# Kernel tuning notes

Measured on AMD Instinct MI355X. Metric: run time of the kernel, lower is better.

Reference implementation:

```python
import jax, jax.numpy as jnp
import numpy as np

DIM = 1024
HEADS = 16
DIM_HEAD = 64
INNER = HEADS * DIM_HEAD
SEQ = 4096
BATCH = 1


def setup_inputs() -> dict:
    key = jax.random.key(0)
    ks = jax.random.split(key, 6)
    s = 0.02
    return {
        "x": jax.random.normal(ks[0], (BATCH, SEQ, DIM), dtype=jnp.float32),
        "Wq": jax.random.normal(ks[1], (DIM, INNER), dtype=jnp.float32) * s,
        "Wk": jax.random.normal(ks[2], (DIM, INNER), dtype=jnp.float32) * s,
        "Wv": jax.random.normal(ks[3], (DIM, INNER), dtype=jnp.float32) * s,
        "Wo": jax.random.normal(ks[4], (INNER, DIM), dtype=jnp.float32) * s,
        "bo": jax.random.normal(ks[5], (DIM,), dtype=jnp.float32) * s,
    }


def reference(x, Wq, Wk, Wv, Wo, bo):
    b, n, _ = x.shape
    beta = 1.0 / jnp.sqrt(jnp.float32(DIM_HEAD))
    # project and split heads: [b, n, inner] -> [b, h, n, d]
    def split_heads(t):
        return t.reshape(b, n, HEADS, DIM_HEAD).transpose(0, 2, 1, 3)
    q = split_heads(x @ Wq)
    k = split_heads(x @ Wk)
    v = split_heads(x @ Wv)
    # scaled scores [b, h, n, n]
    scores = jnp.einsum('bhid,bhjd->bhij', q * beta, k)
    mask_value = -jnp.finfo(scores.dtype).max
    causal = jnp.triu(jnp.ones((n, n), dtype=bool), k=1)
    scores = jnp.where(causal, mask_value, scores)
    attn = jax.nn.softmax(scores, axis=-1)
    out = jnp.einsum('bhij,bhjd->bhid', attn, v)
    out = out.transpose(0, 2, 1, 3).reshape(b, n, INNER)
    # output projection (dropout is identity in eval)
    return out @ Wo + bo
```

## Files before the change

### kernel.cpp

```cpp
#include <hip/hip_runtime.h>
#include <hip/hip_bf16.h>
#include <stdint.h>
#include <math.h>

#define SEQ 4096
#define DIM 1024
#define NHEADS 16
#define DHEAD 64
#define INNER 1024

typedef __hip_bfloat16 bf16;
typedef __attribute__((ext_vector_type(8))) short short8;
typedef __attribute__((ext_vector_type(4))) float floatx4;

__device__ __forceinline__ void gll16(const bf16* g, bf16* l) {
    __builtin_amdgcn_global_load_lds(
        (const __attribute__((address_space(1))) unsigned int*)g,
        (__attribute__((address_space(3))) unsigned int*)l,
        16, 0, 0);
}

__device__ __forceinline__ unsigned short f2bf_bits(float f) {
    bf16 h = __float2bfloat16(f);
    return *reinterpret_cast<unsigned short*>(&h);
}

__device__ __forceinline__ uint2 pack4bf(float a, float b, float c, float d) {
    __hip_bfloat162 lo = __float22bfloat162_rn(float2{a, b});
    __hip_bfloat162 hi = __float22bfloat162_rn(float2{c, d});
    uint2 r;
    r.x = *reinterpret_cast<unsigned*>(&lo);
    r.y = *reinterpret_cast<unsigned*>(&hi);
    return r;
}

__global__ __launch_bounds__(256) void prep_kernel(
        const float* __restrict__ x, const float* __restrict__ W0,
        const float* __restrict__ W1, const float* __restrict__ W2,
        const float* __restrict__ W3, bf16* __restrict__ xb,
        bf16* __restrict__ T0, bf16* __restrict__ T1,
        bf16* __restrict__ T2, bf16* __restrict__ T3) {
    const int tid = threadIdx.x + threadIdx.y * blockDim.x;
    if (blockIdx.z == 4) {
        int chunk = blockIdx.y * 32 + blockIdx.x;
        int base = chunk * 4096 + tid * 4;
        #pragma unroll
        for (int r = 0; r < 4; r++) {
            int i = base + r * 1024;
            float4 f = *reinterpret_cast<const float4*>(x + i);
            unsigned long long p = (unsigned long long)f2bf_bits(f.x)
                                 | ((unsigned long long)f2bf_bits(f.y) << 16)
                                 | ((unsigned long long)f2bf_bits(f.z) << 32)
                                 | ((unsigned long long)f2bf_bits(f.w) << 48);
            *reinterpret_cast<unsigned long long*>(xb + i) = p;
        }
        return;
    }
    const float* W; bf16* T;
    switch (blockIdx.z) {
        case 0:  W = W0; T = T0; break;
        case 1:  W = W1; T = T1; break;
        case 2:  W = W2; T = T2; break;
        default: W = W3; T = T3; break;
    }
    __shared__ float tile[32][33];
    int k0 = blockIdx.x * 32, n0 = blockIdx.y * 32;
    int tx = threadIdx.x, ty = threadIdx.y;
    #pragma unroll
    for (int i = 0; i < 4; i++)
        tile[ty + 8 * i][tx] = W[(size_t)(k0 + ty + 8 * i) * 1024 + n0 + tx];
    __syncthreads();
    #pragma unroll
    for (int i = 0; i < 4; i++)
        T[(size_t)(n0 + ty + 8 * i) * 1024 + k0 + tx] = __float2bfloat16(tile[tx][ty + 8 * i]);
}

__device__ __forceinline__ void gemm128_body(const bf16* __restrict__ A,
                                             const bf16* __restrict__ Bt,
                                             int m0, int n0, floatx4 acc[4][4]) {
    __shared__ __align__(16) bf16 As[8192];
    __shared__ __align__(16) bf16 Bs[8192];
    const int tid = threadIdx.x;
    const int wave = tid >> 6;
    const int lane = tid & 63;
    const int l15 = lane & 15;
    const int quad = lane >> 4;

    #pragma unroll
    for (int i = 0; i < 4; i++)
        #pragma unroll
        for (int j = 0; j < 4; j++)
            acc[i][j] = (floatx4){0.f, 0.f, 0.f, 0.f};

    for (int k0 = 0; k0 < 1024; k0 += 64) {
        __syncthreads();
        #pragma unroll
        for (int j = 0; j < 4; j++) {
            int t = wave * 4 + j;
            int row = (t >> 1) * 16 + l15;
            int kb = (t & 1) * 32 + quad * 8;
            gll16(A + (size_t)(m0 + row) * 1024 + k0 + kb, &As[t * 512]);
            gll16(Bt + (size_t)(n0 + row) * 1024 + k0 + kb, &Bs[t * 512]);
        }
        __syncthreads();
        #pragma unroll
        for (int ks = 0; ks < 2; ks++) {
            short8 af[4], bfr[4];
            #pragma unroll
            for (int i = 0; i < 4; i++)
                af[i] = *reinterpret_cast<const short8*>(
                    &As[((((wave >> 1) * 4 + i) * 2 + ks) * 512) + lane * 8]);
            #pragma unroll
            for (int j = 0; j < 4; j++)
                bfr[j] = *reinterpret_cast<const short8*>(
                    &Bs[((((wave & 1) * 4 + j) * 2 + ks) * 512) + lane * 8]);
            #pragma unroll
            for (int i = 0; i < 4; i++)
                #pragma unroll
                for (int j = 0; j < 4; j++)
                    acc[i][j] = __builtin_amdgcn_mfma_f32_16x16x32_bf16(af[i], bfr[j], acc[i][j], 0, 0, 0);
        }
    }
}

__global__ __launch_bounds__(256) void qkv_gemm_kernel(
        const bf16* __restrict__ xb,
        const bf16* __restrict__ Wqt, const bf16* __restrict__ Wkt, const bf16* __restrict__ Wvt,
        bf16* __restrict__ Qh, bf16* __restrict__ Kh, bf16* __restrict__ Vt) {
    const bf16* Bt;
    if (blockIdx.z == 0)      Bt = Wqt;
    else if (blockIdx.z == 1) Bt = Wkt;
    else                      Bt = Wvt;
    int n0 = blockIdx.x * 128, m0 = blockIdx.y * 128;
    floatx4 acc[4][4];
    gemm128_body(xb, Bt, m0, n0, acc);

    const int tid = threadIdx.x, wave = tid >> 6, lane = tid & 63;
    const int l15 = lane & 15, quad = lane >> 4;
    const int wm = (wave >> 1) * 64, wn = (wave & 1) * 64;
    if (blockIdx.z == 2) {
        #pragma unroll
        for (int i = 0; i < 4; i++)
            #pragma unroll
            for (int j = 0; j < 4; j++) {
                int col = n0 + wn + j * 16 + l15;
                int h = col >> 6, d = col & 63;
                int row0 = m0 + wm + i * 16 + quad * 4;
                uint2 v = pack4bf(acc[i][j][0], acc[i][j][1], acc[i][j][2], acc[i][j][3]);
                *reinterpret_cast<uint2*>(Vt + ((size_t)h * DHEAD + d) * SEQ + row0) = v;
            }
    } else {
        bf16* O = (blockIdx.z == 0) ? Qh : Kh;
        float scale = (blockIdx.z == 0) ? 0.125f * 1.4426950408889634f : 1.0f;
        #pragma unroll
        for (int i = 0; i < 4; i++)
            #pragma unroll
            for (int j = 0; j < 4; j++) {
                int col = n0 + wn + j * 16 + l15;
                int h = col >> 6, d = col & 63;
                #pragma unroll
                for (int r = 0; r < 4; r++) {
                    int row = m0 + wm + i * 16 + quad * 4 + r;
                    O[((size_t)h * SEQ + row) * DHEAD + d] = __float2bfloat16(acc[i][j][r] * scale);
                }
            }
    }
}

__global__ __launch_bounds__(256) void out_gemm_kernel(
        const bf16* __restrict__ Oa, const bf16* __restrict__ Wot,
        const float* __restrict__ bo, float* __restrict__ out) {
    int n0 = blockIdx.x * 128, m0 = blockIdx.y * 128;
    floatx4 acc[4][4];
    gemm128_body(Oa, Wot, m0, n0, acc);

    const int tid = threadIdx.x, wave = tid >> 6, lane = tid & 63;
    const int l15 = lane & 15, quad = lane >> 4;
    const int wm = (wave >> 1) * 64, wn = (wave & 1) * 64;
    #pragma unroll
    for (int i = 0; i < 4; i++)
        #pragma unroll
        for (int j = 0; j < 4; j++) {
            int col = n0 + wn + j * 16 + l15;
            float b = bo[col];
            #pragma unroll
            for (int r = 0; r < 4; r++) {
                int row = m0 + wm + i * 16 + quad * 4 + r;
                out[(size_t)row * DIM + col] = acc[i][j][r] + b;
            }
        }
}

__global__ __launch_bounds__(256, 4) void attention_kernel(
        const bf16* __restrict__ Qh, const bf16* __restrict__ Kh,
        const bf16* __restrict__ Vt, bf16* __restrict__ Oa,
        float* __restrict__ Op0, float* __restrict__ Op1,
        float* __restrict__ L0, float* __restrict__ L1) {
    __shared__ __align__(16) bf16 Ksh[2][4096];
    __shared__ __align__(16) bf16 Vsh[2][4096];
    __shared__ __align__(16) bf16 Ps[4][1024];
    const int tid = threadIdx.x, wave = tid >> 6, lane = tid & 63;
    const int l15 = lane & 15, quad = lane >> 4;
    const int id = blockIdx.x;
    const int head = id & 15;
    const int rk = id >> 4;
    int qt, ck;
    if (rk < 32) { qt = 32 + rk; ck = 0; }
    else {
        int j = rk - 32, pair = j >> 1;
        if ((j & 1) == 0) { qt = 63 - pair; ck = 1; }
        else              { qt = 31 - pair; ck = 0; }
    }
    const int ktile0 = ck ? 32 : 0;
    const int ktile1 = (qt < 32) ? (qt + 1) : (ck ? (qt + 1) : 32);
    const int qw = qt * 64 + wave * 16;
    const size_t hoff = (size_t)head * SEQ * DHEAD;
    const bf16* Qb = Qh + hoff;
    const bf16* Kb = Kh + hoff;
    const bf16* Vb = Vt + hoff;

    short8 bq[2];
    #pragma unroll
    for (int s = 0; s < 2; s++)
        bq[s] = *reinterpret_cast<const short8*>(
            Qb + (size_t)(qw + l15) * DHEAD + s * 32 + quad * 8);

    floatx4 acc_o[4];
    #pragma unroll
    for (int c = 0; c < 4; c++) acc_o[c] = (floatx4){0.f, 0.f, 0.f, 0.f};
    float l_part = 0.f;

    auto stage = [&](int buf, int kbase) {
        #pragma unroll
        for (int j = 0; j < 2; j++) {
            int t = wave * 2 + j;
            gll16(Kb + (size_t)(kbase + (t >> 1) * 16 + l15) * DHEAD + (t & 1) * 32 + quad * 8,
                  &Ksh[buf][t * 512]);
            gll16(Vb + (size_t)((t >> 1) * 16 + l15) * SEQ + kbase + (t & 1) * 32 + quad * 8,
                  &Vsh[buf][t * 512]);
        }
    };

    stage(0, ktile0 * 64);
    __syncthreads();
    int cur = 0;
    for (int kt = ktile0; kt < ktile1; kt++) {
        const int kbase = kt * 64;
        if (kt + 1 < ktile1) stage(cur ^ 1, (kt + 1) * 64);

        floatx4 st[4];
        #pragma unroll
        for (int c = 0; c < 4; c++) st[c] = (floatx4){0.f, 0.f, 0.f, 0.f};
        __builtin_amdgcn_s_setprio(1);
        #pragma unroll
        for (int c = 0; c < 4; c++) {
            short8 ak0 = *reinterpret_cast<const short8*>(&Ksh[cur][(c * 2 + 0) * 512 + lane * 8]);
            short8 ak1 = *reinterpret_cast<const short8*>(&Ksh[cur][(c * 2 + 1) * 512 + lane * 8]);
            st[c] = __builtin_amdgcn_mfma_f32_16x16x32_bf16(ak0, bq[0], st[c], 0, 0, 0);
            st[c] = __builtin_amdgcn_mfma_f32_16x16x32_bf16(ak1, bq[1], st[c], 0, 0, 0);
        }
        __builtin_amdgcn_s_setprio(0);
        if (kbase + 63 > qw) {
            int base0 = kbase + quad * 4 - qw - l15;
            #pragma unroll
            for (int c = 0; c < 4; c++) {
                int base = base0 + c * 16;
                #pragma unroll
                for (int r = 0; r < 4; r++)
                    if (base + r > 0) st[c][r] = -1e30f;
            }
        }
        #pragma unroll
        for (int c = 0; c < 4; c++) {
            float p0 = __builtin_amdgcn_exp2f(st[c][0]);
            float p1 = __builtin_amdgcn_exp2f(st[c][1]);
            float p2 = __builtin_amdgcn_exp2f(st[c][2]);
            float p3 = __builtin_amdgcn_exp2f(st[c][3]);
            l_part += (p0 + p1) + (p2 + p3);
            int elem = (c >> 1) * 512
                     + (l15 + 16 * ((c & 1) * 2 + (quad >> 1))) * 8 + (quad & 1) * 4;
            *reinterpret_cast<uint2*>(&Ps[wave][elem]) = pack4bf(p0, p1, p2, p3);
        }
        __builtin_amdgcn_s_setprio(1);
        #pragma unroll
        for (int s = 0; s < 2; s++) {
            short8 bp = *reinterpret_cast<const short8*>(&Ps[wave][s * 512 + lane * 8]);
            #pragma unroll
            for (int c = 0; c < 4; c++) {
                short8 av = *reinterpret_cast<const short8*>(&Vsh[cur][(c * 2 + s) * 512 + lane * 8]);
                acc_o[c] = __builtin_amdgcn_mfma_f32_16x16x32_bf16(av, bp, acc_o[c], 0, 0, 0);
            }
        }
        __builtin_amdgcn_s_setprio(0);

        __syncthreads();
        cur ^= 1;
    }
    float l = l_part;
    l += __shfl_xor(l, 16, 64);
    l += __shfl_xor(l, 32, 64);
    const int q = qw + l15;
    if (qt < 32) {
        float rcp = 1.0f / l;
        #pragma unroll
        for (int c = 0; c < 4; c++) {
            uint2 v = pack4bf(acc_o[c][0] * rcp, acc_o[c][1] * rcp,
                              acc_o[c][2] * rcp, acc_o[c][3] * rcp);
            *reinterpret_cast<uint2*>(Oa + (size_t)q * INNER + head * DHEAD + c * 16 + quad * 4) = v;
        }
    } else {
        float* Op = ck ? Op1 : Op0;
        float* Lp = ck ? L1 : L0;
        if (quad == 0) Lp[head * 2048 + (q - 2048)] = l;
        #pragma unroll
        for (int c = 0; c < 4; c++)
            *reinterpret_cast<floatx4*>(
                Op + (size_t)(q - 2048) * INNER + head * DHEAD + c * 16 + quad * 4) = acc_o[c];
    }
}

__global__ __launch_bounds__(256) void combine_kernel(
        const float* __restrict__ Op0, const float* __restrict__ Op1,
        const float* __restrict__ L0, const float* __restrict__ L1,
        bf16* __restrict__ Oa) {
    int idx = blockIdx.x * 256 + threadIdx.x;
    int row = idx >> 8;
    int c4 = (idx & 255) * 4;
    int head = c4 >> 6;
    float l = L0[head * 2048 + row] + L1[head * 2048 + row];
    float rcp = 1.0f / l;
    float4 a = *reinterpret_cast<const float4*>(Op0 + (size_t)row * INNER + c4);
    float4 b = *reinterpret_cast<const float4*>(Op1 + (size_t)row * INNER + c4);
    uint2 v = pack4bf((a.x + b.x) * rcp, (a.y + b.y) * rcp,
                      (a.z + b.z) * rcp, (a.w + b.w) * rcp);
    *reinterpret_cast<uint2*>(Oa + (size_t)(2048 + row) * INNER + c4) = v;
}

extern "C" void kernel_launch(void* const* d_in, const int* in_sizes, int n_in,
                              void* d_out, int out_size, void* d_ws, size_t ws_size,
                              hipStream_t stream) {
    const float* x  = (const float*)d_in[0];
    const float* Wq = (const float*)d_in[1];
    const float* Wk = (const float*)d_in[2];
    const float* Wv = (const float*)d_in[3];
    const float* Wo = (const float*)d_in[4];
    const float* bo = (const float*)d_in[5];
    float* out = (float*)d_out;

    char* ws = (char*)d_ws;
    size_t off = 0;
    bf16* xb  = (bf16*)(ws + off); off += (size_t)SEQ * DIM * 2;
    bf16* Wqt = (bf16*)(ws + off); off += (size_t)DIM * INNER * 2;
    bf16* Wkt = (bf16*)(ws + off); off += (size_t)DIM * INNER * 2;
    bf16* Wvt = (bf16*)(ws + off); off += (size_t)DIM * INNER * 2;
    bf16* Wot = (bf16*)(ws + off); off += (size_t)INNER * DIM * 2;
    bf16* Qh  = (bf16*)(ws + off); off += (size_t)NHEADS * SEQ * DHEAD * 2;
    bf16* Kh  = (bf16*)(ws + off); off += (size_t)NHEADS * SEQ * DHEAD * 2;
    bf16* Vtr = (bf16*)(ws + off); off += (size_t)NHEADS * DHEAD * SEQ * 2;
    bf16* Oa  = (bf16*)(ws + off); off += (size_t)SEQ * INNER * 2;
    float* Op0 = (float*)(ws + off); off += (size_t)(SEQ / 2) * INNER * 4;
    float* Op1 = (float*)(ws + off); off += (size_t)(SEQ / 2) * INNER * 4;
    float* L0  = (float*)(ws + off); off += (size_t)NHEADS * (SEQ / 2) * 4;
    float* L1  = (float*)(ws + off); off += (size_t)NHEADS * (SEQ / 2) * 4;

    prep_kernel<<<dim3(32, 32, 5), dim3(32, 8), 0, stream>>>(x, Wq, Wk, Wv, Wo,
                                                             xb, Wqt, Wkt, Wvt, Wot);
    qkv_gemm_kernel<<<dim3(8, 32, 3), 256, 0, stream>>>(xb, Wqt, Wkt, Wvt, Qh, Kh, Vtr);
    attention_kernel<<<1536, 256, 0, stream>>>(Qh, Kh, Vtr, Oa, Op0, Op1, L0, L1);
    combine_kernel<<<2048, 256, 0, stream>>>(Op0, Op1, L0, L1, Oa);
    out_gemm_kernel<<<dim3(8, 32), 256, 0, stream>>>(Oa, Wot, bo, out);
}
```

Measured before the change: 249.9 us.

## Split attention waves into 2 query groups x 2 key halves with LDS reduction

Each wave now handles 32 query rows (two 16-row groups) against half of the 64-key tile, instead of 16 rows against all 64 keys. Each K and V fragment loaded from LDS now feeds two MFMAs, halving LDS read traffic per MFMA for the score and PV products. The cost is partial O and l accumulators that must be summed across key-half wave pairs at the end through shared memory with extra barriers, plus higher register use from doubled accumulators.

```diff
diff --git a/kernel.cpp b/kernel.cpp
--- a/kernel.cpp
+++ b/kernel.cpp
@@ -196,11 +196,14 @@
         const bf16* __restrict__ Vt, bf16* __restrict__ Oa,
         float* __restrict__ Op0, float* __restrict__ Op1,
         float* __restrict__ L0, float* __restrict__ L1) {
-    __shared__ __align__(16) bf16 Ksh[2][4096];
-    __shared__ __align__(16) bf16 Vsh[2][4096];
-    __shared__ __align__(16) bf16 Ps[4][1024];
+    __shared__ __align__(16) char smem[40960];
+    bf16* Kshb = (bf16*)smem;
+    bf16* Vshb = (bf16*)(smem + 16384);
+    bf16* Psb  = (bf16*)(smem + 32768);
     const int tid = threadIdx.x, wave = tid >> 6, lane = tid & 63;
     const int l15 = lane & 15, quad = lane >> 4;
+    const int kp = wave & 1;
+    const int pr = wave >> 1;
     const int id = blockIdx.x;
     const int head = id & 15;
     const int rk = id >> 4;
@@ -213,31 +216,35 @@
     }
     const int ktile0 = ck ? 32 : 0;
     const int ktile1 = (qt < 32) ? (qt + 1) : (ck ? (qt + 1) : 32);
-    const int qw = qt * 64 + wave * 16;
+    const int qw = qt * 64 + pr * 32;
     const size_t hoff = (size_t)head * SEQ * DHEAD;
     const bf16* Qb = Qh + hoff;
     const bf16* Kb = Kh + hoff;
     const bf16* Vb = Vt + hoff;
 
-    short8 bq[2];
-    #pragma unroll
-    for (int s = 0; s < 2; s++)
-        bq[s] = *reinterpret_cast<const short8*>(
-            Qb + (size_t)(qw + l15) * DHEAD + s * 32 + quad * 8);
-
-    floatx4 acc_o[4];
-    #pragma unroll
-    for (int c = 0; c < 4; c++) acc_o[c] = (floatx4){0.f, 0.f, 0.f, 0.f};
-    float l_part = 0.f;
+    short8 bq[2][2];
+    #pragma unroll
+    for (int g = 0; g < 2; g++)
+        #pragma unroll
+        for (int s = 0; s < 2; s++)
+            bq[g][s] = *reinterpret_cast<const short8*>(
+                Qb + (size_t)(qw + g * 16 + l15) * DHEAD + s * 32 + quad * 8);
+
+    floatx4 acc_o[2][4];
+    #pragma unroll
+    for (int g = 0; g < 2; g++)
+        #pragma unroll
+        for (int c = 0; c < 4; c++) acc_o[g][c] = (floatx4){0.f, 0.f, 0.f, 0.f};
+    float l_part[2] = {0.f, 0.f};
 
     auto stage = [&](int buf, int kbase) {
         #pragma unroll
         for (int j = 0; j < 2; j++) {
             int t = wave * 2 + j;
             gll16(Kb + (size_t)(kbase + (t >> 1) * 16 + l15) * DHEAD + (t & 1) * 32 + quad * 8,
-                  &Ksh[buf][t * 512]);
+                  &Kshb[buf * 4096 + t * 512]);
             gll16(Vb + (size_t)((t >> 1) * 16 + l15) * SEQ + kbase + (t & 1) * 32 + quad * 8,
-                  &Vsh[buf][t * 512]);
+                  &Vshb[buf * 4096 + t * 512]);
         }
     };
 
@@ -248,47 +255,59 @@
         const int kbase = kt * 64;
         if (kt + 1 < ktile1) stage(cur ^ 1, (kt + 1) * 64);
 
-        floatx4 st[4];
-        #pragma unroll
-        for (int c = 0; c < 4; c++) st[c] = (floatx4){0.f, 0.f, 0.f, 0.f};
+        floatx4 st[2][2];
+        #pragma unroll
+        for (int g = 0; g < 2; g++)
+            #pragma unroll
+            for (int kg = 0; kg < 2; kg++) st[g][kg] = (floatx4){0.f, 0.f, 0.f, 0.f};
         __builtin_amdgcn_s_setprio(1);
         #pragma unroll
-        for (int c = 0; c < 4; c++) {
-            short8 ak0 = *reinterpret_cast<const short8*>(&Ksh[cur][(c * 2 + 0) * 512 + lane * 8]);
-            short8 ak1 = *reinterpret_cast<const short8*>(&Ksh[cur][(c * 2 + 1) * 512 + lane * 8]);
-            st[c] = __builtin_amdgcn_mfma_f32_16x16x32_bf16(ak0, bq[0], st[c], 0, 0, 0);
-            st[c] = __builtin_amdgcn_mfma_f32_16x16x32_bf16(ak1, bq[1], st[c], 0, 0, 0);
+        for (int kg = 0; kg < 2; kg++) {
+            short8 ak0 = *reinterpret_cast<const short8*>(
+                &Kshb[cur * 4096 + ((kp * 2 + kg) * 2 + 0) * 512 + lane * 8]);
+            short8 ak1 = *reinterpret_cast<const short8*>(
+                &Kshb[cur * 4096 + ((kp * 2 + kg) * 2 + 1) * 512 + lane * 8]);
+            st[0][kg] = __builtin_amdgcn_mfma_f32_16x16x32_bf16(ak0, bq[0][0], st[0][kg], 0, 0, 0);
+            st[0][kg] = __builtin_amdgcn_mfma_f32_16x16x32_bf16(ak1, bq[0][1], st[0][kg], 0, 0, 0);
+            st[1][kg] = __builtin_amdgcn_mfma_f32_16x16x32_bf16(ak0, bq[1][0], st[1][kg], 0, 0, 0);
+            st[1][kg] = __builtin_amdgcn_mfma_f32_16x16x32_bf16(ak1, bq[1][1], st[1][kg], 0, 0, 0);
         }
         __builtin_amdgcn_s_setprio(0);
-        if (kbase + 63 > qw) {
-            int base0 = kbase + quad * 4 - qw - l15;
+        #pragma unroll
+        for (int g = 0; g < 2; g++) {
+            if (kbase + kp * 32 + 31 > qw + g * 16) {
+                int base0 = kbase + kp * 32 + quad * 4 - (qw + g * 16) - l15;
+                #pragma unroll
+                for (int kg = 0; kg < 2; kg++) {
+                    int base = base0 + kg * 16;
+                    #pragma unroll
+                    for (int r = 0; r < 4; r++)
+                        if (base + r > 0) st[g][kg][r] = -1e30f;
+                }
+            }
+        }
+        #pragma unroll
+        for (int g = 0; g < 2; g++)
+            #pragma unroll
+            for (int kg = 0; kg < 2; kg++) {
+                float p0 = __builtin_amdgcn_exp2f(st[g][kg][0]);
+                float p1 = __builtin_amdgcn_exp2f(st[g][kg][1]);
+                float p2 = __builtin_amdgcn_exp2f(st[g][kg][2]);
+                float p3 = __builtin_amdgcn_exp2f(st[g][kg][3]);
+                l_part[g] += (p0 + p1) + (p2 + p3);
+                int elem = g * 512 + (l15 + 16 * (kg * 2 + (quad >> 1))) * 8 + (quad & 1) * 4;
+                *reinterpret_cast<uint2*>(&Psb[wave * 1024 + elem]) = pack4bf(p0, p1, p2, p3);
+            }
+        __builtin_amdgcn_s_setprio(1);
+        {
+            short8 bp0 = *reinterpret_cast<const short8*>(&Psb[wave * 1024 + 0 * 512 + lane * 8]);
+            short8 bp1 = *reinterpret_cast<const short8*>(&Psb[wave * 1024 + 1 * 512 + lane * 8]);
             #pragma unroll
             for (int c = 0; c < 4; c++) {
-                int base = base0 + c * 16;
-                #pragma unroll
-                for (int r = 0; r < 4; r++)
-                    if (base + r > 0) st[c][r] = -1e30f;
-            }
-        }
-        #pragma unroll
-        for (int c = 0; c < 4; c++) {
-            float p0 = __builtin_amdgcn_exp2f(st[c][0]);
-            float p1 = __builtin_amdgcn_exp2f(st[c][1]);
-            float p2 = __builtin_amdgcn_exp2f(st[c][2]);
-            float p3 = __builtin_amdgcn_exp2f(st[c][3]);
-            l_part += (p0 + p1) + (p2 + p3);
-            int elem = (c >> 1) * 512
-                     + (l15 + 16 * ((c & 1) * 2 + (quad >> 1))) * 8 + (quad & 1) * 4;
-            *reinterpret_cast<uint2*>(&Ps[wave][elem]) = pack4bf(p0, p1, p2, p3);
-        }
-        __builtin_amdgcn_s_setprio(1);
-        #pragma unroll
-        for (int s = 0; s < 2; s++) {
-            short8 bp = *reinterpret_cast<const short8*>(&Ps[wave][s * 512 + lane * 8]);
-            #pragma unroll
-            for (int c = 0; c < 4; c++) {
-                short8 av = *reinterpret_cast<const short8*>(&Vsh[cur][(c * 2 + s) * 512 + lane * 8]);
-                acc_o[c] = __builtin_amdgcn_mfma_f32_16x16x32_bf16(av, bp, acc_o[c], 0, 0, 0);
+                short8 av = *reinterpret_cast<const short8*>(
+                    &Vshb[cur * 4096 + (c * 2 + kp) * 512 + lane * 8]);
+                acc_o[0][c] = __builtin_amdgcn_mfma_f32_16x16x32_bf16(av, bp0, acc_o[0][c], 0, 0, 0);
+                acc_o[1][c] = __builtin_amdgcn_mfma_f32_16x16x32_bf16(av, bp1, acc_o[1][c], 0, 0, 0);
             }
         }
         __builtin_amdgcn_s_setprio(0);
@@ -296,26 +315,62 @@
         __syncthreads();
         cur ^= 1;
     }
-    float l = l_part;
-    l += __shfl_xor(l, 16, 64);
-    l += __shfl_xor(l, 32, 64);
-    const int q = qw + l15;
-    if (qt < 32) {
-        float rcp = 1.0f / l;
-        #pragma unroll
-        for (int c = 0; c < 4; c++) {
-            uint2 v = pack4bf(acc_o[c][0] * rcp, acc_o[c][1] * rcp,
-                              acc_o[c][2] * rcp, acc_o[c][3] * rcp);
-            *reinterpret_cast<uint2*>(Oa + (size_t)q * INNER + head * DHEAD + c * 16 + quad * 4) = v;
-        }
-    } else {
-        float* Op = ck ? Op1 : Op0;
-        float* Lp = ck ? L1 : L0;
-        if (quad == 0) Lp[head * 2048 + (q - 2048)] = l;
-        #pragma unroll
-        for (int c = 0; c < 4; c++)
-            *reinterpret_cast<floatx4*>(
-                Op + (size_t)(q - 2048) * INNER + head * DHEAD + c * 16 + quad * 4) = acc_o[c];
+    float lv[2];
+    #pragma unroll
+    for (int g = 0; g < 2; g++) {
+        float l = l_part[g];
+        l += __shfl_xor(l, 16, 64);
+        l += __shfl_xor(l, 32, 64);
+        lv[g] = l;
+    }
+    __syncthreads();
+    floatx4* Red = (floatx4*)smem;
+    float* Lred = (float*)(smem + 32768);
+    if (kp == 1) {
+        #pragma unroll
+        for (int g = 0; g < 2; g++)
+            #pragma unroll
+            for (int c = 0; c < 4; c++)
+                Red[pr * 512 + (g * 4 + c) * 64 + lane] = acc_o[g][c];
+        if (quad == 0) {
+            Lred[pr * 32 + l15] = lv[0];
+            Lred[pr * 32 + 16 + l15] = lv[1];
+        }
+    }
+    __syncthreads();
+    if (kp == 0) {
+        #pragma unroll
+        for (int g = 0; g < 2; g++)
+            #pragma unroll
+            for (int c = 0; c < 4; c++) {
+                floatx4 o = Red[pr * 512 + (g * 4 + c) * 64 + lane];
+                acc_o[g][c][0] += o[0]; acc_o[g][c][1] += o[1];
+                acc_o[g][c][2] += o[2]; acc_o[g][c][3] += o[3];
+            }
+        lv[0] += Lred[pr * 32 + l15];
+        lv[1] += Lred[pr * 32 + 16 + l15];
+        #pragma unroll
+        for (int g = 0; g < 2; g++) {
+            const int q = qw + g * 16 + l15;
+            if (qt < 32) {
+                float rcp = 1.0f / lv[g];
+                #pragma unroll
+                for (int c = 0; c < 4; c++) {
+                    uint2 v = pack4bf(acc_o[g][c][0] * rcp, acc_o[g][c][1] * rcp,
+                                      acc_o[g][c][2] * rcp, acc_o[g][c][3] * rcp);
+                    *reinterpret_cast<uint2*>(
+                        Oa + (size_t)q * INNER + head * DHEAD + c * 16 + quad * 4) = v;
+                }
+            } else {
+                float* Op = ck ? Op1 : Op0;
+                float* Lp = ck ? L1 : L0;
+                if (quad == 0) Lp[head * 2048 + (q - 2048)] = lv[g];
+                #pragma unroll
+                for (int c = 0; c < 4; c++)
+                    *reinterpret_cast<floatx4*>(
+                        Op + (size_t)(q - 2048) * INNER + head * DHEAD + c * 16 + quad * 4) = acc_o[g][c];
+            }
+        }
     }
 }
 
```

Result: slower. 259.8 us (+4.0%).

## Use 32x32 MFMA in attention with register-resident P via permlane swap

Applied to the files above, without the earlier changes.

Rewrites the attention kernel to use 32x32x16 bf16 MFMAs with 32 query rows per wave and 128-row query tiles. The softmax probabilities stay in registers and are reshaped into the B operand with v_permlane32_swap, which removes the LDS round-trip for P and its shared buffer. The grid is halved and the causal split/work assignment is remapped to the larger tiles. Fewer, larger MFMAs and no P staging should cut LDS traffic and instruction overhead. The cost is more register pressure, fewer blocks for load balance, and more masked wasted work on diagonal tiles.

```diff
diff --git a/kernel.cpp b/kernel.cpp
--- a/kernel.cpp
+++ b/kernel.cpp
@@ -12,6 +12,7 @@
 typedef __hip_bfloat16 bf16;
 typedef __attribute__((ext_vector_type(8))) short short8;
 typedef __attribute__((ext_vector_type(4))) float floatx4;
+typedef __attribute__((ext_vector_type(16))) float floatx16;
 
 __device__ __forceinline__ void gll16(const bf16* g, bf16* l) {
     __builtin_amdgcn_global_load_lds(
@@ -32,6 +33,11 @@
     r.x = *reinterpret_cast<unsigned*>(&lo);
     r.y = *reinterpret_cast<unsigned*>(&hi);
     return r;
+}
+
+__device__ __forceinline__ unsigned pkbf(float lo, float hi) {
+    __hip_bfloat162 h = __float22bfloat162_rn(float2{lo, hi});
+    return *reinterpret_cast<unsigned*>(&h);
 }
 
 __global__ __launch_bounds__(256) void prep_kernel(
@@ -191,6 +197,25 @@
         }
 }
 
+#define PV_STEP(P, KTG)                                                              \
+    do {                                                                             \
+        const int rb_ = ((KTG) & 1) * 8;                                             \
+        unsigned A0_ = pkbf((P)[rb_ + 0], (P)[rb_ + 1]);                             \
+        unsigned B0_ = pkbf((P)[rb_ + 4], (P)[rb_ + 5]);                             \
+        unsigned A1_ = pkbf((P)[rb_ + 2], (P)[rb_ + 3]);                             \
+        unsigned B1_ = pkbf((P)[rb_ + 6], (P)[rb_ + 7]);                             \
+        asm("v_permlane32_swap_b32 %0, %1" : "+v"(A0_), "+v"(B0_));                  \
+        asm("v_permlane32_swap_b32 %0, %1" : "+v"(A1_), "+v"(B1_));                  \
+        uint4 w_; w_.x = A0_; w_.y = A1_; w_.z = B0_; w_.w = B1_;                    \
+        short8 bp_ = *reinterpret_cast<short8*>(&w_);                                \
+        short8 av0_ = *reinterpret_cast<const short8*>(                              \
+            &Vsh[cur][(KTG) * 512 + lane * 8]);                                      \
+        short8 av1_ = *reinterpret_cast<const short8*>(                              \
+            &Vsh[cur][(4 + (KTG)) * 512 + lane * 8]);                                \
+        acc0 = __builtin_amdgcn_mfma_f32_32x32x16_bf16(av0_, bp_, acc0, 0, 0, 0);    \
+        acc1 = __builtin_amdgcn_mfma_f32_32x32x16_bf16(av1_, bp_, acc1, 0, 0, 0);    \
+    } while (0)
+
 __global__ __launch_bounds__(256, 4) void attention_kernel(
         const bf16* __restrict__ Qh, const bf16* __restrict__ Kh,
         const bf16* __restrict__ Vt, bf16* __restrict__ Oa,
@@ -198,46 +223,45 @@
         float* __restrict__ L0, float* __restrict__ L1) {
     __shared__ __align__(16) bf16 Ksh[2][4096];
     __shared__ __align__(16) bf16 Vsh[2][4096];
-    __shared__ __align__(16) bf16 Ps[4][1024];
     const int tid = threadIdx.x, wave = tid >> 6, lane = tid & 63;
-    const int l15 = lane & 15, quad = lane >> 4;
+    const int ql = lane & 31, half = lane >> 5;
+    const int h8 = half * 8;
     const int id = blockIdx.x;
     const int head = id & 15;
     const int rk = id >> 4;
-    int qt, ck;
-    if (rk < 32) { qt = 32 + rk; ck = 0; }
-    else {
-        int j = rk - 32, pair = j >> 1;
-        if ((j & 1) == 0) { qt = 63 - pair; ck = 1; }
-        else              { qt = 31 - pair; ck = 0; }
-    }
-    const int ktile0 = ck ? 32 : 0;
-    const int ktile1 = (qt < 32) ? (qt + 1) : (ck ? (qt + 1) : 32);
-    const int qw = qt * 64 + wave * 16;
+    int t, ck;
+    if (rk < 16)      { t = 16 + rk; ck = 0; }
+    else if (rk < 32) { t = 47 - rk; ck = 1; }
+    else              { t = 47 - rk; ck = 0; }
+    const bool split = (t >= 16);
+    const int ktile0 = (split && ck == 1) ? 32 : 0;
+    const int ktile1 = (split && ck == 0) ? 32 : (2 * t + 2);
+    const int qw = t * 128 + wave * 32;
+    const int q = qw + ql;
     const size_t hoff = (size_t)head * SEQ * DHEAD;
     const bf16* Qb = Qh + hoff;
     const bf16* Kb = Kh + hoff;
     const bf16* Vb = Vt + hoff;
 
-    short8 bq[2];
-    #pragma unroll
-    for (int s = 0; s < 2; s++)
-        bq[s] = *reinterpret_cast<const short8*>(
-            Qb + (size_t)(qw + l15) * DHEAD + s * 32 + quad * 8);
-
-    floatx4 acc_o[4];
-    #pragma unroll
-    for (int c = 0; c < 4; c++) acc_o[c] = (floatx4){0.f, 0.f, 0.f, 0.f};
+    short8 bq[4];
+    #pragma unroll
+    for (int kc = 0; kc < 4; kc++)
+        bq[kc] = *reinterpret_cast<const short8*>(
+            Qb + (size_t)q * DHEAD + kc * 16 + h8);
+
+    floatx16 acc0, acc1;
+    #pragma unroll
+    for (int r = 0; r < 16; r++) { acc0[r] = 0.f; acc1[r] = 0.f; }
     float l_part = 0.f;
 
     auto stage = [&](int buf, int kbase) {
         #pragma unroll
         for (int j = 0; j < 2; j++) {
-            int t = wave * 2 + j;
-            gll16(Kb + (size_t)(kbase + (t >> 1) * 16 + l15) * DHEAD + (t & 1) * 32 + quad * 8,
-                  &Ksh[buf][t * 512]);
-            gll16(Vb + (size_t)((t >> 1) * 16 + l15) * SEQ + kbase + (t & 1) * 32 + quad * 8,
-                  &Vsh[buf][t * 512]);
+            int tc = wave * 2 + j;
+            gll16(Kb + (size_t)(kbase + (tc >> 2) * 32 + ql) * DHEAD + (tc & 3) * 16 + h8,
+                  &Ksh[buf][tc * 512]);
+            gll16(Vb + (size_t)((tc >> 2) * 32 + ql) * SEQ + kbase + (tc & 3) * 16 + h8,
+                  &Vsh[buf][tc * 512]);
         }
     };
 
@@ -248,74 +272,67 @@
         const int kbase = kt * 64;
         if (kt + 1 < ktile1) stage(cur ^ 1, (kt + 1) * 64);
 
-        floatx4 st[4];
-        #pragma unroll
-        for (int c = 0; c < 4; c++) st[c] = (floatx4){0.f, 0.f, 0.f, 0.f};
+        floatx16 s0, s1;
+        #pragma unroll
+        for (int r = 0; r < 16; r++) { s0[r] = 0.f; s1[r] = 0.f; }
         __builtin_amdgcn_s_setprio(1);
         #pragma unroll
-        for (int c = 0; c < 4; c++) {
-            short8 ak0 = *reinterpret_cast<const short8*>(&Ksh[cur][(c * 2 + 0) * 512 + lane * 8]);
-            short8 ak1 = *reinterpret_cast<const short8*>(&Ksh[cur][(c * 2 + 1) * 512 + lane * 8]);
-            st[c] = __builtin_amdgcn_mfma_f32_16x16x32_bf16(ak0, bq[0], st[c], 0, 0, 0);
-            st[c] = __builtin_amdgcn_mfma_f32_16x16x32_bf16(ak1, bq[1], st[c], 0, 0, 0);
+        for (int kc = 0; kc < 4; kc++) {
+            short8 ak0 = *reinterpret_cast<const short8*>(&Ksh[cur][kc * 512 + lane * 8]);
+            short8 ak1 = *reinterpret_cast<const short8*>(&Ksh[cur][(4 + kc) * 512 + lane * 8]);
+            s0 = __builtin_amdgcn_mfma_f32_32x32x16_bf16(ak0, bq[kc], s0, 0, 0, 0);
+            s1 = __builtin_amdgcn_mfma_f32_32x32x16_bf16(ak1, bq[kc], s1, 0, 0, 0);
         }
         __builtin_amdgcn_s_setprio(0);
         if (kbase + 63 > qw) {
-            int base0 = kbase + quad * 4 - qw - l15;
-            #pragma unroll
-            for (int c = 0; c < 4; c++) {
-                int base = base0 + c * 16;
-                #pragma unroll
-                for (int r = 0; r < 4; r++)
-                    if (base + r > 0) st[c][r] = -1e30f;
+            int base0 = kbase + half * 4 - q;
+            #pragma unroll
+            for (int r = 0; r < 16; r++) {
+                int off = (r & 3) + 8 * (r >> 2);
+                if (base0 + off > 0)      s0[r] = -1e30f;
+                if (base0 + 32 + off > 0) s1[r] = -1e30f;
             }
         }
         #pragma unroll
-        for (int c = 0; c < 4; c++) {
-            float p0 = __builtin_amdgcn_exp2f(st[c][0]);
-            float p1 = __builtin_amdgcn_exp2f(st[c][1]);
-            float p2 = __builtin_amdgcn_exp2f(st[c][2]);
-            float p3 = __builtin_amdgcn_exp2f(st[c][3]);
-            l_part += (p0 + p1) + (p2 + p3);
-            int elem = (c >> 1) * 512
-                     + (l15 + 16 * ((c & 1) * 2 + (quad >> 1))) * 8 + (quad & 1) * 4;
-            *reinterpret_cast<uint2*>(&Ps[wave][elem]) = pack4bf(p0, p1, p2, p3);
+        for (int r = 0; r < 16; r++) {
+            s0[r] = __builtin_amdgcn_exp2f(s0[r]);
+            s1[r] = __builtin_amdgcn_exp2f(s1[r]);
+            l_part += s0[r] + s1[r];
         }
         __builtin_amdgcn_s_setprio(1);
-        #pragma unroll
-        for (int s = 0; s < 2; s++) {
-            short8 bp = *reinterpret_cast<const short8*>(&Ps[wave][s * 512 + lane * 8]);
-            #pragma unroll
-            for (int c = 0; c < 4; c++) {
-                short8 av = *reinterpret_cast<const short8*>(&Vsh[cur][(c * 2 + s) * 512 + lane * 8]);
-                acc_o[c] = __builtin_amdgcn_mfma_f32_16x16x32_bf16(av, bp, acc_o[c], 0, 0, 0);
-            }
-        }
+        PV_STEP(s0, 0); PV_STEP(s0, 1); PV_STEP(s1, 2); PV_STEP(s1, 3);
         __builtin_amdgcn_s_setprio(0);
 
         __syncthreads();
         cur ^= 1;
     }
-    float l = l_part;
-    l += __shfl_xor(l, 16, 64);
-    l += __shfl_xor(l, 32, 64);
-    const int q = qw + l15;
-    if (qt < 32) {
+    float l = l_part + __shfl_xor(l_part, 32, 64);
+    if (!split) {
         float rcp = 1.0f / l;
         #pragma unroll
-        for (int c = 0; c < 4; c++) {
-            uint2 v = pack4bf(acc_o[c][0] * rcp, acc_o[c][1] * rcp,
-                              acc_o[c][2] * rcp, acc_o[c][3] * rcp);
-            *reinterpret_cast<uint2*>(Oa + (size_t)q * INNER + head * DHEAD + c * 16 + quad * 4) = v;
+        for (int a = 0; a < 4; a++) {
+            int d0 = 8 * a + half * 4;
+            uint2 v0 = pack4bf(acc0[4 * a + 0] * rcp, acc0[4 * a + 1] * rcp,
+                               acc0[4 * a + 2] * rcp, acc0[4 * a + 3] * rcp);
+            *reinterpret_cast<uint2*>(Oa + (size_t)q * INNER + head * DHEAD + d0) = v0;
+            uint2 v1 = pack4bf(acc1[4 * a + 0] * rcp, acc1[4 * a + 1] * rcp,
+                               acc1[4 * a + 2] * rcp, acc1[4 * a + 3] * rcp);
+            *reinterpret_cast<uint2*>(Oa + (size_t)q * INNER + head * DHEAD + 32 + d0) = v1;
         }
     } else {
         float* Op = ck ? Op1 : Op0;
         float* Lp = ck ? L1 : L0;
-        if (quad == 0) Lp[head * 2048 + (q - 2048)] = l;
-        #pragma unroll
-        for (int c = 0; c < 4; c++)
+        if (half == 0) Lp[head * 2048 + (q - 2048)] = l;
+        #pragma unroll
+        for (int a = 0; a < 4; a++) {
+            int d0 = 8 * a + half * 4;
+            floatx4 v0 = {acc0[4 * a + 0], acc0[4 * a + 1], acc0[4 * a + 2], acc0[4 * a + 3]};
             *reinterpret_cast<floatx4*>(
-                Op + (size_t)(q - 2048) * INNER + head * DHEAD + c * 16 + quad * 4) = acc_o[c];
+                Op + (size_t)(q - 2048) * INNER + head * DHEAD + d0) = v0;
+            floatx4 v1 = {acc1[4 * a + 0], acc1[4 * a + 1], acc1[4 * a + 2], acc1[4 * a + 3]};
+            *reinterpret_cast<floatx4*>(
+                Op + (size_t)(q - 2048) * INNER + head * DHEAD + 32 + d0) = v1;
+        }
     }
 }
 
@@ -366,7 +383,7 @@
     prep_kernel<<<dim3(32, 32, 5), dim3(32, 8), 0, stream>>>(x, Wq, Wk, Wv, Wo,
                                                              xb, Wqt, Wkt, Wvt, Wot);
     qkv_gemm_kernel<<<dim3(8, 32, 3), 256, 0, stream>>>(xb, Wqt, Wkt, Wvt, Qh, Kh, Vtr);
-    attention_kernel<<<1536, 256, 0, stream>>>(Qh, Kh, Vtr, Oa, Op0, Op1, L0, L1);
+    attention_kernel<<<768, 256, 0, stream>>>(Qh, Kh, Vtr, Oa, Op0, Op1, L0, L1);
     combine_kernel<<<2048, 256, 0, stream>>>(Op0, Op1, L0, L1, Oa);
     out_gemm_kernel<<<dim3(8, 32), 256, 0, stream>>>(Oa, Wot, bo, out);
 }
```

New measurement: 248.5 us. No clear change (-0.6%).
